# Kernel tuning notes

Measured on AMD Instinct MI355X. Metric: run time of the kernel, lower is better.

The kernel has to match this reference:

```python
import jax, jax.numpy as jnp
import numpy as np

B, L, H, D = 64, 2048, 1024, 128  # segments, segment length, hidden, input_dim
N = B * L

def swish(z):
    return z * jax.nn.sigmoid(z)

def setup_inputs() -> dict:
    key = jax.random.key(0)
    ks = jax.random.split(key, 10)
    s = 0.02
    x_seeds = jax.random.normal(ks[0], (N, D), dtype=jnp.float32)
    x_nodes = jax.random.normal(ks[1], (N, D), dtype=jnp.float32)
    W_seed = jax.random.normal(ks[2], (H, D), dtype=jnp.float32) * s
    W_node = jax.random.normal(ks[3], (H, D), dtype=jnp.float32) * s
    W1 = jax.random.normal(ks[4], (H, H), dtype=jnp.float32) * s
    b1 = jnp.zeros((H,), dtype=jnp.float32)
    W2 = jax.random.normal(ks[5], (H, H), dtype=jnp.float32) * s
    b2 = jnp.zeros((H,), dtype=jnp.float32)
    w_ns = jax.random.normal(ks[6], (1, H), dtype=jnp.float32) * s   # node_score_layer (zero-init in src; random for nontrivial baseline)
    W_stop = jax.random.normal(ks[7], (2, H), dtype=jnp.float32) * s  # stopping_score_layer
    starts = jnp.arange(B, dtype=jnp.int32) * L
    indptr = jnp.stack([starts, starts + L, starts + L], axis=1)  # (start, end, candidate_end)
    return {"x_seeds": x_seeds, "x_nodes": x_nodes, "W_seed": W_seed, "W_node": W_node,
            "W1": W1, "b1": b1, "W2": W2, "b2": b2, "w_ns": w_ns, "W_stop": W_stop,
            "indptr": indptr}

def reference(x_seeds, x_nodes, W_seed, W_node, W1, b1, W2, b2, w_ns, W_stop, indptr):
    # embeddings + 2-layer Swish MLP
    h = x_seeds @ W_seed.T + x_nodes @ W_node.T            # [N, H]
    h = swish(h @ W1.T + b1)
    h = swish(h @ W2.T + b2)
    node_scores = (h @ w_ns.T)[:, 0]                       # [N]
    # ragged segments (uniform length L) defined by indptr starts
    nb = indptr.shape[0]
    seg_len = h.shape[0] // nb                             # static L
    idx = indptr[:, 0][:, None] + jnp.arange(seg_len)      # [B, L]
    h_seg = h[idx]                                         # [B, L, H]
    stop_node = h_seg.mean(axis=1)                         # [B, H] per-segment mean pool
    node_logits = jax.nn.log_softmax(node_scores[idx], axis=1)          # [B, L]
    stop_logits = jax.nn.log_softmax(stop_node @ W_stop.T, axis=1)      # [B, 2]
    # concat([node_logits + stop0, stop1]) per segment
    return jnp.concatenate([node_logits + stop_logits[:, :1], stop_logits[:, 1:]], axis=1)  # [B, L+1]
```

## Files before the change

kernel.cpp:

```cpp
#include <hip/hip_runtime.h>

typedef float f32x4 __attribute__((ext_vector_type(4)));
typedef __bf16 bf16x8 __attribute__((ext_vector_type(8)));
typedef unsigned short u16x8 __attribute__((ext_vector_type(8)));

#define DEVINL static __device__ __forceinline__

DEVINL unsigned short f2bf(float f) {
    unsigned int u = __builtin_bit_cast(unsigned int, f);
    u += 0x7fffu + ((u >> 16) & 1u);
    return (unsigned short)(u >> 16);
}
DEVINL float bf2f(unsigned short u) {
    unsigned int x = ((unsigned int)u) << 16;
    return __builtin_bit_cast(float, x);
}

#define GLD16(gp, lp)                                                          \
    __builtin_amdgcn_global_load_lds(                                          \
        (const __attribute__((address_space(1))) void*)(gp),                   \
        (__attribute__((address_space(3))) void*)(lp), 16, 0, 0)

__global__ void pack_cat_k(const float* __restrict__ s0, const float* __restrict__ s1,
                           unsigned short* __restrict__ dst, int nchunks) {
    int e = blockIdx.x * 256 + threadIdx.x;
    if (e >= nchunks) return;
    int row = e >> 5, ch = e & 31;
    const float* src = (ch < 16) ? (s0 + (size_t)row * 128 + ch * 8)
                                 : (s1 + (size_t)row * 128 + (ch - 16) * 8);
    float4 a = *(const float4*)src;
    float4 b = *(const float4*)(src + 4);
    u16x8 o;
    o[0] = f2bf(a.x); o[1] = f2bf(a.y); o[2] = f2bf(a.z); o[3] = f2bf(a.w);
    o[4] = f2bf(b.x); o[5] = f2bf(b.y); o[6] = f2bf(b.z); o[7] = f2bf(b.w);
    *(u16x8*)(dst + (size_t)e * 8) = o;
}

__global__ void cvt_k(const float* __restrict__ s, unsigned short* __restrict__ d, int nchunks) {
    int e = blockIdx.x * 256 + threadIdx.x;
    if (e >= nchunks) return;
    float4 a = *(const float4*)(s + (size_t)e * 8);
    float4 b = *(const float4*)(s + (size_t)e * 8 + 4);
    u16x8 o;
    o[0] = f2bf(a.x); o[1] = f2bf(a.y); o[2] = f2bf(a.z); o[3] = f2bf(a.w);
    o[4] = f2bf(b.x); o[5] = f2bf(b.y); o[6] = f2bf(b.z); o[7] = f2bf(b.w);
    *(u16x8*)(d + (size_t)e * 8) = o;
}

template <int EPI>
__global__ void gemm_bt_k(const unsigned short* __restrict__ A,
                          const unsigned short* __restrict__ B,
                          const float* __restrict__ bias,
                          unsigned short* __restrict__ C,
                          int M, int N, int K) {
    __shared__ unsigned short As[128 * 32];
    __shared__ unsigned short Bs[128 * 32];
    const int tid  = threadIdx.x;
    const int lane = tid & 63;
    const int wv   = tid >> 6;
    const int wr   = wv >> 1, wc = wv & 1;
    const int ntn  = N >> 7;

    const int nwg = gridDim.x;
    const int xcd = blockIdx.x & 7, blk = blockIdx.x >> 3;
    const int q = nwg >> 3, rr = nwg & 7;
    const int logical = (xcd < rr ? xcd * (q + 1) : rr * (q + 1) + (xcd - rr) * q) + blk;

    const int im   = logical / ntn, in = logical % ntn;
    const size_t rowA0 = (size_t)im * 128, rowB0 = (size_t)in * 128;

    const int e0 = tid, e1 = tid + 256;
    const int ra0 = e0 >> 2, ca0 = (e0 & 3) * 8;
    const int ra1 = e1 >> 2, ca1 = (e1 & 3) * 8;

    f32x4 acc[4][4] = {};
    const int frow = lane & 15;
    const int kb   = (lane >> 4) * 8;

    for (int k0 = 0; k0 < K; k0 += 32) {
        GLD16(A + (rowA0 + ra0) * K + k0 + ca0, (char*)As + e0 * 16);
        GLD16(A + (rowA0 + ra1) * K + k0 + ca1, (char*)As + e1 * 16);
        GLD16(B + (rowB0 + ra0) * K + k0 + ca0, (char*)Bs + e0 * 16);
        GLD16(B + (rowB0 + ra1) * K + k0 + ca1, (char*)Bs + e1 * 16);
        __syncthreads();

        bf16x8 af[4], bfr[4];
#pragma unroll
        for (int m = 0; m < 4; ++m)
            af[m] = *(const bf16x8*)&As[(wr * 64 + m * 16 + frow) * 32 + kb];
#pragma unroll
        for (int n = 0; n < 4; ++n)
            bfr[n] = *(const bf16x8*)&Bs[(wc * 64 + n * 16 + frow) * 32 + kb];
#pragma unroll
        for (int m = 0; m < 4; ++m)
#pragma unroll
            for (int n = 0; n < 4; ++n)
                acc[m][n] = __builtin_amdgcn_mfma_f32_16x16x32_bf16(af[m], bfr[n], acc[m][n], 0, 0, 0);
        __syncthreads();
    }

    const int r4 = (lane >> 4) * 4;
    const int cc = lane & 15;
#pragma unroll
    for (int n = 0; n < 4; ++n) {
        const int col = (int)rowB0 + wc * 64 + n * 16 + cc;
        const float bv = (EPI == 1) ? bias[col] : 0.0f;
#pragma unroll
        for (int m = 0; m < 4; ++m) {
            const size_t row = rowA0 + wr * 64 + m * 16 + r4;
#pragma unroll
            for (int r = 0; r < 4; ++r) {
                float v = acc[m][n][r] + bv;
                if (EPI == 1) v = v / (1.0f + __expf(-v));
                C[(row + r) * (size_t)N + col] = f2bf(v);
            }
        }
    }
}

DEVINL int swz16(int b) { return b ^ (((b >> 7) & 7) << 4); }

template <int W>
DEVINL void vmw() {
    if constexpr (W == 8) asm volatile("s_waitcnt vmcnt(8)" ::: "memory");
    else if constexpr (W == 4) asm volatile("s_waitcnt vmcnt(4)" ::: "memory");
    else if constexpr (W == 0) asm volatile("s_waitcnt vmcnt(0)" ::: "memory");
}

template <int MH, int NH, int W, typename F>
DEVINL void qphase(char* smA, char* smB, int p, f32x4 (&acc)[8][4],
                   int wr, int wc, int fr, int kg, F&& stg) {
    char* Ab = smA + p * 32768 + MH * 16384;
    char* Bb = smB + p * 32768 + NH * 16384;
    bf16x8 aF[4][2], bF[2][2];
#pragma unroll
    for (int m2 = 0; m2 < 4; ++m2)
#pragma unroll
        for (int kk = 0; kk < 2; ++kk)
            aF[m2][kk] = *(const bf16x8*)(Ab + swz16((wr * 64 + m2 * 16 + fr) * 128 + kk * 64 + kg));
#pragma unroll
    for (int n2 = 0; n2 < 2; ++n2)
#pragma unroll
        for (int kk = 0; kk < 2; ++kk)
            bF[n2][kk] = *(const bf16x8*)(Bb + swz16((wc * 32 + n2 * 16 + fr) * 128 + kk * 64 + kg));
    stg();
    vmw<W>();
    __builtin_amdgcn_s_barrier();
    __builtin_amdgcn_s_setprio(1);
#pragma unroll
    for (int kk = 0; kk < 2; ++kk)
#pragma unroll
        for (int m2 = 0; m2 < 4; ++m2)
#pragma unroll
            for (int n2 = 0; n2 < 2; ++n2)
                acc[MH * 4 + m2][NH * 2 + n2] = __builtin_amdgcn_mfma_f32_16x16x32_bf16(
                    aF[m2][kk], bF[n2][kk], acc[MH * 4 + m2][NH * 2 + n2], 0, 0, 0);
    __builtin_amdgcn_s_setprio(0);
    __builtin_amdgcn_s_barrier();
}

template <int EPI>
__launch_bounds__(512, 1)
__global__ void gemm256_k(const unsigned short* __restrict__ A,
                          const unsigned short* __restrict__ Bm,
                          const float* __restrict__ bias,
                          unsigned short* __restrict__ C,
                          const float* __restrict__ wns,
                          float* __restrict__ sc,
                          float* __restrict__ pl,
                          int M, int N, int K) {
    extern __shared__ __align__(16) char sm[];
    char* smA = sm;
    char* smB = sm + 65536;
    const int tid  = threadIdx.x;
    const int lane = tid & 63, w = tid >> 6;
    const int wr = w >> 2, wc = w & 3;
    const int fr = lane & 15;
    const int kg = (lane >> 4) * 16;
    const int ntn = N >> 8;

    const int nwg = gridDim.x;
    const int xcd = blockIdx.x & 7, blk = blockIdx.x >> 3;
    const int q = nwg >> 3, rr = nwg & 7;
    const int logical = (xcd < rr ? xcd * (q + 1) : rr * (q + 1) + (xcd - rr) * q) + blk;
    const int im = logical / ntn, in = logical % ntn;
    const size_t rowA0 = (size_t)im * 256, colB0 = (size_t)in * 256;
    const int NT = K >> 6;

    f32x4 acc[8][4] = {};

    auto stageA = [&](int tile, int half, int par) {
#pragma unroll
        for (int j = 0; j < 2; ++j) {
            const int c = tid + j * 512;
            const int gc = (c & 7) ^ ((c >> 3) & 7);
            GLD16(A + (rowA0 + half * 128 + (c >> 3)) * K + tile * 64 + gc * 8,
                  smA + par * 32768 + half * 16384 + c * 16);
        }
    };
    auto stageB = [&](int tile, int half, int par) {
#pragma unroll
        for (int j = 0; j < 2; ++j) {
            const int c = tid + j * 512;
            const int gc = (c & 7) ^ ((c >> 3) & 7);
            GLD16(Bm + (colB0 + half * 128 + (c >> 3)) * K + tile * 64 + gc * 8,
                  smB + par * 32768 + half * 16384 + c * 16);
        }
    };
    auto nop = [] {};

    stageA(0, 0, 0); stageB(0, 0, 0);
    stageB(0, 1, 0); stageA(0, 1, 0);
    stageA(1, 0, 1); stageB(1, 0, 1);
    vmw<8>();
    __builtin_amdgcn_s_barrier();

    for (int t = 0; t + 2 < NT; ++t) {
        const int p = t & 1;
        qphase<0, 0, 8>(smA, smB, p, acc, wr, wc, fr, kg, [&] { stageB(t + 1, 1, p ^ 1); });
        qphase<0, 1, 8>(smA, smB, p, acc, wr, wc, fr, kg, [&] { stageA(t + 1, 1, p ^ 1); });
        qphase<1, 0, 8>(smA, smB, p, acc, wr, wc, fr, kg, [&] { stageA(t + 2, 0, p); });
        qphase<1, 1, 8>(smA, smB, p, acc, wr, wc, fr, kg, [&] { stageB(t + 2, 0, p); });
    }
    {
        const int t = NT - 2, p = t & 1;
        qphase<0, 0, 8>(smA, smB, p, acc, wr, wc, fr, kg, [&] { stageB(t + 1, 1, p ^ 1); });
        qphase<0, 1, 8>(smA, smB, p, acc, wr, wc, fr, kg, [&] { stageA(t + 1, 1, p ^ 1); });
        qphase<1, 0, 4>(smA, smB, p, acc, wr, wc, fr, kg, nop);
        qphase<1, 1, 0>(smA, smB, p, acc, wr, wc, fr, kg, nop);
    }
    {
        const int p = (NT - 1) & 1;
        qphase<0, 0, -1>(smA, smB, p, acc, wr, wc, fr, kg, nop);
        qphase<0, 1, -1>(smA, smB, p, acc, wr, wc, fr, kg, nop);
        qphase<1, 0, -1>(smA, smB, p, acc, wr, wc, fr, kg, nop);
        qphase<1, 1, -1>(smA, smB, p, acc, wr, wc, fr, kg, nop);
    }

    const int r4 = (lane >> 4) * 4;
    const int cc = lane & 15;

    if (EPI == 2) {
#pragma unroll
        for (int n = 0; n < 4; ++n) {
            const float bv = bias[(int)colB0 + (n >> 1) * 128 + wc * 32 + (n & 1) * 16 + cc];
#pragma unroll
            for (int m = 0; m < 8; ++m)
#pragma unroll
                for (int r = 0; r < 4; ++r) {
                    float v = acc[m][n][r] + bv;
                    acc[m][n][r] = v / (1.0f + __expf(-v));
                }
        }
#pragma unroll
        for (int m = 0; m < 8; ++m)
#pragma unroll
            for (int r = 0; r < 4; ++r) {
                float s = 0.f;
#pragma unroll
                for (int n = 0; n < 4; ++n)
                    s += acc[m][n][r] * wns[(int)colB0 + (n >> 1) * 128 + wc * 32 + (n & 1) * 16 + cc];
#pragma unroll
                for (int o = 1; o < 16; o <<= 1) s += __shfl_xor(s, o);
                if (cc == 0)
                    atomicAdd(&sc[rowA0 + (m >> 2) * 128 + wr * 64 + (m & 3) * 16 + r4 + r], s);
            }
        const int seg = (int)(rowA0 >> 11);
#pragma unroll
        for (int n = 0; n < 4; ++n) {
            float p2 = 0.f;
#pragma unroll
            for (int m = 0; m < 8; ++m)
#pragma unroll
                for (int r = 0; r < 4; ++r) p2 += acc[m][n][r];
            p2 += __shfl_xor(p2, 16);
            p2 += __shfl_xor(p2, 32);
            if ((lane >> 4) == 0)
                atomicAdd(&pl[seg * 1024 + (int)colB0 + (n >> 1) * 128 + wc * 32 + (n & 1) * 16 + cc],
                          p2 * (1.0f / 2048.0f));
        }
        return;
    }

#pragma unroll
    for (int n = 0; n < 4; ++n) {
        const int col = (int)colB0 + (n >> 1) * 128 + wc * 32 + (n & 1) * 16 + cc;
        const float bv = bias[col];
#pragma unroll
        for (int m = 0; m < 8; ++m) {
            const size_t row = rowA0 + (m >> 2) * 128 + wr * 64 + (m & 3) * 16 + r4;
#pragma unroll
            for (int r = 0; r < 4; ++r) {
                float v = acc[m][n][r] + bv;
                v = v / (1.0f + __expf(-v));
                C[(row + r) * (size_t)N + col] = f2bf(v);
            }
        }
    }
}

__global__ void stop_k(const float* __restrict__ pool, const float* __restrict__ Wstop,
                       float* __restrict__ stp, float* __restrict__ out) {
    const int b = blockIdx.x, t = threadIdx.x;
    float a0 = 0.f, a1 = 0.f;
#pragma unroll
    for (int j = 0; j < 4; ++j) {
        const int hcol = t + j * 256;
        const float pv = pool[b * 1024 + hcol];
        a0 += pv * Wstop[hcol];
        a1 += pv * Wstop[1024 + hcol];
    }
    const int lane = t & 63, wv = t >> 6;
#pragma unroll
    for (int off = 32; off; off >>= 1) { a0 += __shfl_down(a0, off); a1 += __shfl_down(a1, off); }
    __shared__ float r0[4], r1[4];
    if (lane == 0) { r0[wv] = a0; r1[wv] = a1; }
    __syncthreads();
    if (t == 0) {
        const float s0 = r0[0] + r0[1] + r0[2] + r0[3];
        const float s1 = r1[0] + r1[1] + r1[2] + r1[3];
        const float m  = fmaxf(s0, s1);
        const float lse = m + __logf(__expf(s0 - m) + __expf(s1 - m));
        stp[b * 2] = s0 - lse;
        out[(size_t)b * 2049 + 2048] = s1 - lse;
    }
}

__global__ void node_k(const float* __restrict__ sc, const float* __restrict__ stp,
                       float* __restrict__ out) {
    const int b = blockIdx.x, t = threadIdx.x;
    const float* s = sc + (size_t)b * 2048;
    float v[8];
    float mx = -3.4e38f;
#pragma unroll
    for (int j = 0; j < 8; ++j) { v[j] = s[t + j * 256]; mx = fmaxf(mx, v[j]); }
    const int lane = t & 63, wv = t >> 6;
    __shared__ float red[4];
#pragma unroll
    for (int off = 32; off; off >>= 1) mx = fmaxf(mx, __shfl_down(mx, off));
    if (lane == 0) red[wv] = mx;
    __syncthreads();
    mx = fmaxf(fmaxf(red[0], red[1]), fmaxf(red[2], red[3]));
    float se = 0.f;
#pragma unroll
    for (int j = 0; j < 8; ++j) se += __expf(v[j] - mx);
    __syncthreads();
#pragma unroll
    for (int off = 32; off; off >>= 1) se += __shfl_down(se, off);
    if (lane == 0) red[wv] = se;
    __syncthreads();
    se = red[0] + red[1] + red[2] + red[3];
    const float base = stp[b * 2] - mx - __logf(se);
#pragma unroll
    for (int j = 0; j < 8; ++j) out[(size_t)b * 2049 + t + j * 256] = v[j] + base;
}

extern "C" void kernel_launch(void* const* d_in, const int* in_sizes, int n_in,
                              void* d_out, int out_size, void* d_ws, size_t ws_size,
                              hipStream_t stream) {
    (void)in_sizes; (void)n_in; (void)out_size;
    const float* x_seeds = (const float*)d_in[0];
    const float* x_nodes = (const float*)d_in[1];
    const float* W_seed  = (const float*)d_in[2];
    const float* W_node  = (const float*)d_in[3];
    const float* W1      = (const float*)d_in[4];
    const float* b1      = (const float*)d_in[5];
    const float* W2      = (const float*)d_in[6];
    const float* b2      = (const float*)d_in[7];
    const float* w_ns    = (const float*)d_in[8];
    const float* W_stop  = (const float*)d_in[9];
    float* out = (float*)d_out;

    const int N = 131072, H = 1024, B = 64;

    {
        auto f1 = gemm256_k<1>; auto f2 = gemm256_k<2>;
        hipFuncSetAttribute((const void*)f1, hipFuncAttributeMaxDynamicSharedMemorySize, 131072);
        hipFuncSetAttribute((const void*)f2, hipFuncAttributeMaxDynamicSharedMemorySize, 131072);
    }

    char* ws = (char*)d_ws;
    size_t off = 0;
    auto alloc = [&](size_t bytes) {
        char* p = ws + off;
        off += (bytes + 255) & ~(size_t)255;
        return p;
    };
    unsigned short* wcat = (unsigned short*)alloc((size_t)H * 256 * 2);
    unsigned short* W1b  = (unsigned short*)alloc((size_t)H * H * 2);
    unsigned short* W2b  = (unsigned short*)alloc((size_t)H * H * 2);
    float* scores = (float*)alloc((size_t)N * 4);
    float* pool   = (float*)alloc((size_t)B * H * 4);
    float* stp    = (float*)alloc((size_t)B * 2 * 4);

    const size_t per_row = 256 * 2 + 1024 * 2 + 1024 * 2;
    size_t avail = (ws_size > off + (1u << 20)) ? (ws_size - off - (1u << 20)) : 0;
    long long mc_ll = (long long)(avail / per_row) / 2048 * 2048;
    int Mc = (int)(mc_ll < 2048 ? 2048 : (mc_ll > 65536 ? 65536 : mc_ll));

    unsigned short* xcat_c = (unsigned short*)alloc((size_t)Mc * 256 * 2);
    unsigned short* h0_c   = (unsigned short*)alloc((size_t)Mc * H * 2);
    unsigned short* h1_c   = (unsigned short*)alloc((size_t)Mc * H * 2);

    hipMemsetAsync(pool, 0, (size_t)B * H * 4, stream);
    hipMemsetAsync(scores, 0, (size_t)N * 4, stream);

    pack_cat_k<<<(H * 32) / 256, 256, 0, stream>>>(W_seed, W_node, wcat, H * 32);
    cvt_k<<<(H * H / 8) / 256, 256, 0, stream>>>(W1, W1b, H * H / 8);
    cvt_k<<<(H * H / 8) / 256, 256, 0, stream>>>(W2, W2b, H * H / 8);

    for (int base = 0; base < N; base += Mc) {
        const int m = (N - base < Mc) ? (N - base) : Mc;
        pack_cat_k<<<(m * 32) / 256, 256, 0, stream>>>(
            x_seeds + (size_t)base * 128, x_nodes + (size_t)base * 128, xcat_c, m * 32);
        const int grid128 = (m / 128) * (H / 128);
        gemm_bt_k<0><<<grid128, 256, 0, stream>>>(xcat_c, wcat, nullptr, h0_c, m, H, 256);
        const int grid256 = (m / 256) * (H / 256);
        gemm256_k<1><<<grid256, 512, 131072, stream>>>(h0_c, W1b, b1, h1_c,
                                                       nullptr, nullptr, nullptr, m, H, H);
        gemm256_k<2><<<grid256, 512, 131072, stream>>>(h1_c, W2b, b2, nullptr,
                                                       w_ns, scores + base,
                                                       pool + (size_t)(base / 2048) * H, m, H, H);
    }

    stop_k<<<B, 256, 0, stream>>>(pool, W_stop, stp, out);
    node_k<<<B, 256, 0, stream>>>(scores, stp, out);
}
```

Measured before the change: 1.094 ms.

## Move second GEMM epilogue to 128-tile kernel and restructure 256-tile pipeline waits

The fused swish/score/pool epilogue for the W2 layer moves from the 256x256 tile kernel to the smaller 128x128 gemm_bt kernel. The 256-tile kernel becomes EPI-1 only, with a compile-time ping-pong parity, loop unrolling by two tiles, and a vmcnt wait only once per tile group instead of every phase. The intent is to cut per-phase wait and barrier overhead in the main GEMM. The risk is that the second GEMM now runs on the simpler, lower-throughput 128 kernel and its staging order was changed, which could hurt or break correctness.

```diff
diff --git a/kernel.cpp b/kernel.cpp
--- a/kernel.cpp
+++ b/kernel.cpp
@@ -52,6 +52,9 @@
                           const unsigned short* __restrict__ B,
                           const float* __restrict__ bias,
                           unsigned short* __restrict__ C,
+                          const float* __restrict__ wns,
+                          float* __restrict__ sc,
+                          float* __restrict__ pl,
                           int M, int N, int K) {
     __shared__ unsigned short As[128 * 32];
     __shared__ unsigned short Bs[128 * 32];
@@ -101,6 +104,49 @@
 
     const int r4 = (lane >> 4) * 4;
     const int cc = lane & 15;
+
+    if (EPI == 2) {
+#pragma unroll
+        for (int n = 0; n < 4; ++n) {
+            const float bv = bias[(int)rowB0 + wc * 64 + n * 16 + cc];
+#pragma unroll
+            for (int m = 0; m < 4; ++m)
+#pragma unroll
+                for (int r = 0; r < 4; ++r) {
+                    float v = acc[m][n][r] + bv;
+                    acc[m][n][r] = v / (1.0f + __expf(-v));
+                }
+        }
+#pragma unroll
+        for (int m = 0; m < 4; ++m)
+#pragma unroll
+            for (int r = 0; r < 4; ++r) {
+                float s = 0.f;
+#pragma unroll
+                for (int n = 0; n < 4; ++n)
+                    s += acc[m][n][r] * wns[(int)rowB0 + wc * 64 + n * 16 + cc];
+#pragma unroll
+                for (int o = 1; o < 16; o <<= 1) s += __shfl_xor(s, o);
+                if (cc == 0)
+                    atomicAdd(&sc[rowA0 + wr * 64 + m * 16 + r4 + r], s);
+            }
+        const int seg = (int)(rowA0 >> 11);
+#pragma unroll
+        for (int n = 0; n < 4; ++n) {
+            float p = 0.f;
+#pragma unroll
+            for (int m = 0; m < 4; ++m)
+#pragma unroll
+                for (int r = 0; r < 4; ++r) p += acc[m][n][r];
+            p += __shfl_xor(p, 16);
+            p += __shfl_xor(p, 32);
+            if ((lane >> 4) == 0)
+                atomicAdd(&pl[seg * 1024 + (int)rowB0 + wc * 64 + n * 16 + cc],
+                          p * (1.0f / 2048.0f));
+        }
+        return;
+    }
+
 #pragma unroll
     for (int n = 0; n < 4; ++n) {
         const int col = (int)rowB0 + wc * 64 + n * 16 + cc;
@@ -127,11 +173,11 @@
     else if constexpr (W == 0) asm volatile("s_waitcnt vmcnt(0)" ::: "memory");
 }
 
-template <int MH, int NH, int W, typename F>
-DEVINL void qphase(char* smA, char* smB, int p, f32x4 (&acc)[8][4],
+template <int P, int MH, int NH, int W, typename F>
+DEVINL void qphase(char* smA, char* smB, f32x4 (&acc)[8][4],
                    int wr, int wc, int fr, int kg, F&& stg) {
-    char* Ab = smA + p * 32768 + MH * 16384;
-    char* Bb = smB + p * 32768 + NH * 16384;
+    char* Ab = smA + P * 32768 + MH * 16384;
+    char* Bb = smB + P * 32768 + NH * 16384;
     bf16x8 aF[4][2], bF[2][2];
 #pragma unroll
     for (int m2 = 0; m2 < 4; ++m2)
@@ -159,15 +205,11 @@
     __builtin_amdgcn_s_barrier();
 }
 
-template <int EPI>
 __launch_bounds__(512, 1)
 __global__ void gemm256_k(const unsigned short* __restrict__ A,
                           const unsigned short* __restrict__ Bm,
                           const float* __restrict__ bias,
                           unsigned short* __restrict__ C,
-                          const float* __restrict__ wns,
-                          float* __restrict__ sc,
-                          float* __restrict__ pl,
                           int M, int N, int K) {
     extern __shared__ __align__(16) char sm[];
     char* smA = sm;
@@ -212,76 +254,36 @@
     stageA(0, 0, 0); stageB(0, 0, 0);
     stageB(0, 1, 0); stageA(0, 1, 0);
     stageA(1, 0, 1); stageB(1, 0, 1);
-    vmw<8>();
+    vmw<4>();
     __builtin_amdgcn_s_barrier();
 
-    for (int t = 0; t + 2 < NT; ++t) {
-        const int p = t & 1;
-        qphase<0, 0, 8>(smA, smB, p, acc, wr, wc, fr, kg, [&] { stageB(t + 1, 1, p ^ 1); });
-        qphase<0, 1, 8>(smA, smB, p, acc, wr, wc, fr, kg, [&] { stageA(t + 1, 1, p ^ 1); });
-        qphase<1, 0, 8>(smA, smB, p, acc, wr, wc, fr, kg, [&] { stageA(t + 2, 0, p); });
-        qphase<1, 1, 8>(smA, smB, p, acc, wr, wc, fr, kg, [&] { stageB(t + 2, 0, p); });
-    }
+#define GRP_STEADY(Pp, tt)                                                           \
+    qphase<Pp, 0, 0, -1>(smA, smB, acc, wr, wc, fr, kg, [&] { stageA(tt + 1, 1, Pp ^ 1); }); \
+    qphase<Pp, 0, 1, -1>(smA, smB, acc, wr, wc, fr, kg, [&] { stageB(tt + 1, 1, Pp ^ 1); }); \
+    qphase<Pp, 1, 0, -1>(smA, smB, acc, wr, wc, fr, kg, [&] { stageA(tt + 2, 0, Pp); });     \
+    qphase<Pp, 1, 1,  4>(smA, smB, acc, wr, wc, fr, kg, [&] { stageB(tt + 2, 0, Pp); });
+
+    for (int t = 0; t + 3 < NT; t += 2) {
+        GRP_STEADY(0, t);
+        GRP_STEADY(1, t + 1);
+    }
+#undef GRP_STEADY
     {
-        const int t = NT - 2, p = t & 1;
-        qphase<0, 0, 8>(smA, smB, p, acc, wr, wc, fr, kg, [&] { stageB(t + 1, 1, p ^ 1); });
-        qphase<0, 1, 8>(smA, smB, p, acc, wr, wc, fr, kg, [&] { stageA(t + 1, 1, p ^ 1); });
-        qphase<1, 0, 4>(smA, smB, p, acc, wr, wc, fr, kg, nop);
-        qphase<1, 1, 0>(smA, smB, p, acc, wr, wc, fr, kg, nop);
+        const int t = NT - 2;
+        qphase<0, 0, 0, -1>(smA, smB, acc, wr, wc, fr, kg, [&] { stageA(t + 1, 1, 1); });
+        qphase<0, 0, 1, -1>(smA, smB, acc, wr, wc, fr, kg, [&] { stageB(t + 1, 1, 1); });
+        qphase<0, 1, 0, -1>(smA, smB, acc, wr, wc, fr, kg, nop);
+        qphase<0, 1, 1,  0>(smA, smB, acc, wr, wc, fr, kg, nop);
     }
     {
-        const int p = (NT - 1) & 1;
-        qphase<0, 0, -1>(smA, smB, p, acc, wr, wc, fr, kg, nop);
-        qphase<0, 1, -1>(smA, smB, p, acc, wr, wc, fr, kg, nop);
-        qphase<1, 0, -1>(smA, smB, p, acc, wr, wc, fr, kg, nop);
-        qphase<1, 1, -1>(smA, smB, p, acc, wr, wc, fr, kg, nop);
+        qphase<1, 0, 0, -1>(smA, smB, acc, wr, wc, fr, kg, nop);
+        qphase<1, 0, 1, -1>(smA, smB, acc, wr, wc, fr, kg, nop);
+        qphase<1, 1, 0, -1>(smA, smB, acc, wr, wc, fr, kg, nop);
+        qphase<1, 1, 1, -1>(smA, smB, acc, wr, wc, fr, kg, nop);
     }
 
     const int r4 = (lane >> 4) * 4;
     const int cc = lane & 15;
-
-    if (EPI == 2) {
-#pragma unroll
-        for (int n = 0; n < 4; ++n) {
-            const float bv = bias[(int)colB0 + (n >> 1) * 128 + wc * 32 + (n & 1) * 16 + cc];
-#pragma unroll
-            for (int m = 0; m < 8; ++m)
-#pragma unroll
-                for (int r = 0; r < 4; ++r) {
-                    float v = acc[m][n][r] + bv;
-                    acc[m][n][r] = v / (1.0f + __expf(-v));
-                }
-        }
-#pragma unroll
-        for (int m = 0; m < 8; ++m)
-#pragma unroll
-            for (int r = 0; r < 4; ++r) {
-                float s = 0.f;
-#pragma unroll
-                for (int n = 0; n < 4; ++n)
-                    s += acc[m][n][r] * wns[(int)colB0 + (n >> 1) * 128 + wc * 32 + (n & 1) * 16 + cc];
-#pragma unroll
-                for (int o = 1; o < 16; o <<= 1) s += __shfl_xor(s, o);
-                if (cc == 0)
-                    atomicAdd(&sc[rowA0 + (m >> 2) * 128 + wr * 64 + (m & 3) * 16 + r4 + r], s);
-            }
-        const int seg = (int)(rowA0 >> 11);
-#pragma unroll
-        for (int n = 0; n < 4; ++n) {
-            float p2 = 0.f;
-#pragma unroll
-            for (int m = 0; m < 8; ++m)
-#pragma unroll
-                for (int r = 0; r < 4; ++r) p2 += acc[m][n][r];
-            p2 += __shfl_xor(p2, 16);
-            p2 += __shfl_xor(p2, 32);
-            if ((lane >> 4) == 0)
-                atomicAdd(&pl[seg * 1024 + (int)colB0 + (n >> 1) * 128 + wc * 32 + (n & 1) * 16 + cc],
-                          p2 * (1.0f / 2048.0f));
-        }
-        return;
-    }
-
 #pragma unroll
     for (int n = 0; n < 4; ++n) {
         const int col = (int)colB0 + (n >> 1) * 128 + wc * 32 + (n & 1) * 16 + cc;
@@ -373,11 +375,8 @@
 
     const int N = 131072, H = 1024, B = 64;
 
-    {
-        auto f1 = gemm256_k<1>; auto f2 = gemm256_k<2>;
-        hipFuncSetAttribute((const void*)f1, hipFuncAttributeMaxDynamicSharedMemorySize, 131072);
-        hipFuncSetAttribute((const void*)f2, hipFuncAttributeMaxDynamicSharedMemorySize, 131072);
-    }
+    hipFuncSetAttribute((const void*)&gemm256_k,
+                        hipFuncAttributeMaxDynamicSharedMemorySize, 131072);
 
     char* ws = (char*)d_ws;
     size_t off = 0;
@@ -414,13 +413,13 @@
         pack_cat_k<<<(m * 32) / 256, 256, 0, stream>>>(
             x_seeds + (size_t)base * 128, x_nodes + (size_t)base * 128, xcat_c, m * 32);
         const int grid128 = (m / 128) * (H / 128);
-        gemm_bt_k<0><<<grid128, 256, 0, stream>>>(xcat_c, wcat, nullptr, h0_c, m, H, 256);
+        gemm_bt_k<0><<<grid128, 256, 0, stream>>>(xcat_c, wcat, nullptr, h0_c,
+                                                  nullptr, nullptr, nullptr, m, H, 256);
         const int grid256 = (m / 256) * (H / 256);
-        gemm256_k<1><<<grid256, 512, 131072, stream>>>(h0_c, W1b, b1, h1_c,
-                                                       nullptr, nullptr, nullptr, m, H, H);
-        gemm256_k<2><<<grid256, 512, 131072, stream>>>(h1_c, W2b, b2, nullptr,
-                                                       w_ns, scores + base,
-                                                       pool + (size_t)(base / 2048) * H, m, H, H);
+        gemm256_k<<<grid256, 512, 131072, stream>>>(h0_c, W1b, b1, h1_c, m, H, H);
+        gemm_bt_k<2><<<grid128, 256, 0, stream>>>(h1_c, W2b, b2, nullptr,
+                                                  w_ns, scores + base,
+                                                  pool + (size_t)(base / 2048) * H, m, H, H);
     }
 
     stop_k<<<B, 256, 0, stream>>>(pool, W_stop, stp, out);
```

Measured after the change: 1.070 ms. -2.2%, faster.
